# Performance work log

Measured on AMD Instinct MI355X. Metric: run time of the kernel, lower is better.

Reference implementation:

```python
import jax, jax.numpy as jnp
import numpy as np

MAX_RADIUS = 0.9
TEMP = 0.1

def _to_poincare(x, W, b):
    # Linear + Tanh, then rescale into Poincare ball of radius 0.9
    h = jnp.tanh(x @ W.T + b)
    norm = jnp.clip(jnp.linalg.norm(h, axis=-1, keepdims=True), 1e-8, None)
    scale = jnp.where(norm > MAX_RADIUS, MAX_RADIUS / norm, jnp.ones_like(norm))
    return h * scale

def setup_inputs() -> dict:
    key = jax.random.key(0)
    kq, kw, kb, km, ko = jax.random.split(key, 5)
    B, N, D = 2048, 100000, 128
    return {
        "query": jax.random.normal(kq, (B, D), dtype=jnp.float32),
        "W": jax.random.normal(kw, (D, D), dtype=jnp.float32) * (1.0 / np.sqrt(D)),
        "b": jax.random.normal(kb, (D,), dtype=jnp.float32) * 0.01,
        "mem_emb": jax.random.normal(km, (N, D), dtype=jnp.float32),
        "mem_out": jax.random.normal(ko, (N, D), dtype=jnp.float32),
        "k": 16,
    }

def reference(query, W, b, mem_emb, mem_out, k):
    q = _to_poincare(query, W, b)          # [B, D]
    m = _to_poincare(mem_emb, W, b)        # [N, D]
    # Euclidean cdist via the GEMM form: ||q||^2 + ||m||^2 - 2 q.m
    q2 = jnp.sum(q * q, axis=-1, keepdims=True)           # [B, 1]
    m2 = jnp.sum(m * m, axis=-1)                          # [N]
    d2 = q2 + m2[None, :] - 2.0 * (q @ m.T)               # [B, N]
    dists = jnp.sqrt(jnp.maximum(d2, 1e-12))
    # k smallest distances
    neg_top, top_idx = jax.lax.top_k(-dists, k)           # [B, k]
    top_dists = -neg_top
    weights = jax.nn.softmax(-top_dists / TEMP, axis=-1)  # [B, k]
    outcomes = mem_out[top_idx]                           # [B, k, D]
    return weights, outcomes
```

## Files before the change

### kernel.cpp

```cpp
#include <hip/hip_runtime.h>
#include <hip/hip_bf16.h>
#include <math.h>

#define DIM 128
#define QB 64
#define MB 128
#define NSPLIT 16
#define KSEL 16
#define KOWN 4
#define RESCORE 32
#define IDXMASK 0x1FFFu
#define KEYMASK 0xFFFFE000u

using bf16x8 = __attribute__((ext_vector_type(8))) short;
using f32x4  = __attribute__((ext_vector_type(4))) float;

__device__ inline unsigned short f2bf(float f) {
  __hip_bfloat16 h = __float2bfloat16(f);
  return __builtin_bit_cast(unsigned short, h);
}

__device__ inline f32x4 mfma16(bf16x8 a, bf16x8 b, f32x4 c) {
  return __builtin_amdgcn_mfma_f32_16x16x32_bf16(a, b, c, 0, 0, 0);
}

__device__ inline void gload_lds16(const void* g, void* l) {
  __builtin_amdgcn_global_load_lds(
      (const __attribute__((address_space(1))) void*)g,
      (__attribute__((address_space(3))) void*)l, 16, 0, 0);
}

__global__ __launch_bounds__(512) void poincare2_k(
    const float* __restrict__ Xm, int Rm,
    const float* __restrict__ Xq, int Rq,
    const float* __restrict__ W, const float* __restrict__ bias,
    float* __restrict__ Pm, float* __restrict__ Pm2,
    unsigned short* __restrict__ Pmbf,
    float* __restrict__ Pq, float* __restrict__ Pq2, int nbm)
{
  __shared__ float Wl[DIM * DIM];
  __shared__ float nrm[128 * 17];
  __shared__ float norm2l[128];

  const int t  = threadIdx.x;
  const int cg = t & 15;
  const int rg = t >> 4;

  const bool ismem = (int)blockIdx.x < nbm;
  const float* X = ismem ? Xm : Xq;
  const int    R = ismem ? Rm : Rq;
  float*       P  = ismem ? Pm  : Pq;
  float*       P2 = ismem ? Pm2 : Pq2;
  unsigned short* Pbf = ismem ? Pmbf : nullptr;
  const int rbase = (ismem ? blockIdx.x : (blockIdx.x - nbm)) * 128;

  for (int i = t; i < DIM * 32; i += 512) {
    const int j = i >> 5, c = i & 31;
    const float4 v = *(const float4*)&W[j * DIM + c * 4];
    *(float4*)&Wl[j * DIM + ((c ^ ((j >> 3) & 7)) << 2)] = v;
  }
  float bj[8];
  #pragma unroll
  for (int u = 0; u < 8; ++u) bj[u] = bias[cg * 8 + u];

  const float* xr[4];
  #pragma unroll
  for (int v = 0; v < 4; ++v) {
    int row = rbase + rg + 32 * v;
    if (row > R - 1) row = R - 1;
    xr[v] = X + (size_t)row * DIM;
  }
  __syncthreads();

  float acc[4][8];
  #pragma unroll
  for (int v = 0; v < 4; ++v)
    #pragma unroll
    for (int u = 0; u < 8; ++u) acc[v][u] = bj[u];

  #pragma unroll 2
  for (int k4 = 0; k4 < 32; ++k4) {
    float4 xv[4], wv[8];
    #pragma unroll
    for (int v = 0; v < 4; ++v) xv[v] = *(const float4*)&xr[v][k4 * 4];
    #pragma unroll
    for (int u = 0; u < 8; ++u) {
      const int j = cg * 8 + u;
      wv[u] = *(const float4*)&Wl[j * DIM + ((k4 ^ ((j >> 3) & 7)) << 2)];
    }
    #pragma unroll
    for (int v = 0; v < 4; ++v)
      #pragma unroll
      for (int u = 0; u < 8; ++u) {
        acc[v][u] = fmaf(xv[v].x, wv[u].x, acc[v][u]);
        acc[v][u] = fmaf(xv[v].y, wv[u].y, acc[v][u]);
        acc[v][u] = fmaf(xv[v].z, wv[u].z, acc[v][u]);
        acc[v][u] = fmaf(xv[v].w, wv[u].w, acc[v][u]);
      }
  }

  #pragma unroll
  for (int v = 0; v < 4; ++v) {
    float pn = 0.f;
    #pragma unroll
    for (int u = 0; u < 8; ++u) {
      const float th = tanhf(acc[v][u]);
      acc[v][u] = th;
      pn = fmaf(th, th, pn);
    }
    nrm[(rg + 32 * v) * 17 + cg] = pn;
  }
  __syncthreads();
  if (t < 128) {
    float s = 0.f;
    #pragma unroll
    for (int c2 = 0; c2 < 16; ++c2) s += nrm[t * 17 + c2];
    norm2l[t] = s;
    if (rbase + t < R) {
      const float nm = sqrtf(s);
      const float sc = (nm > 0.9f) ? (0.9f / nm) : 1.0f;
      P2[rbase + t] = s * sc * sc;
    }
  }
  __syncthreads();

  #pragma unroll
  for (int v = 0; v < 4; ++v) {
    const int r = rg + 32 * v;
    const int row = rbase + r;
    if (row < R) {
      const float n2 = norm2l[r];
      const float nm = sqrtf(n2);
      const float sc = (nm > 0.9f) ? (0.9f / nm) : 1.0f;
      float o[8];
      #pragma unroll
      for (int u = 0; u < 8; ++u) o[u] = acc[v][u] * sc;
      *(float4*)&P[(size_t)row * DIM + cg * 8]     = make_float4(o[0], o[1], o[2], o[3]);
      *(float4*)&P[(size_t)row * DIM + cg * 8 + 4] = make_float4(o[4], o[5], o[6], o[7]);
      if (Pbf) {
        uint4 pb;
        pb.x = (unsigned)f2bf(o[0]) | ((unsigned)f2bf(o[1]) << 16);
        pb.y = (unsigned)f2bf(o[2]) | ((unsigned)f2bf(o[3]) << 16);
        pb.z = (unsigned)f2bf(o[4]) | ((unsigned)f2bf(o[5]) << 16);
        pb.w = (unsigned)f2bf(o[6]) | ((unsigned)f2bf(o[7]) << 16);
        *(uint4*)&Pmbf[(size_t)row * DIM + ((cg ^ (row & 7)) << 3)] = pb;
      }
    }
  }
}

template<bool USEBF>
__global__ __launch_bounds__(512, 4) void score_topk_k(
    const float* __restrict__ Pq,
    const float* __restrict__ Pm, const float* __restrict__ Pm2,
    const unsigned short* __restrict__ Pmbf,
    int N, int splitlen, unsigned* __restrict__ splitTop)
{
  __shared__ __align__(16) unsigned short Ml[2][MB * DIM];
  __shared__ float m2p2l[2][MB];

  const int t = threadIdx.x;
  const int lane = t & 63;
  const int w = t >> 6, wr = w >> 2, wc = w & 3;
  const int split = blockIdx.x;
  const int qbase = blockIdx.y * QB;
  const int mlo = split * splitlen;
  const int mhi = min(mlo + splitlen, N);

  bf16x8 qf[2][4];
  #pragma unroll
  for (int s = 0; s < 2; ++s) {
    const int qrow = qbase + (wr * 2 + s) * 16 + (lane & 15);
    #pragma unroll
    for (int ks = 0; ks < 4; ++ks) {
      const float* src = &Pq[(size_t)qrow * DIM + ks * 32 + (lane >> 4) * 8];
      float4 lo = *(const float4*)src;
      float4 hi = *(const float4*)(src + 4);
      bf16x8 v;
      v[0] = (short)f2bf(lo.x); v[1] = (short)f2bf(lo.y);
      v[2] = (short)f2bf(lo.z); v[3] = (short)f2bf(lo.w);
      v[4] = (short)f2bf(hi.x); v[5] = (short)f2bf(hi.y);
      v[6] = (short)f2bf(hi.z); v[7] = (short)f2bf(hi.w);
      qf[s][ks] = v;
    }
  }

  uint4 sv[4];
  auto stage_issue = [&](int mbase, int buf) {
    if constexpr (USEBF) {
      #pragma unroll
      for (int i = 0; i < 4; ++i) {
        const int rr = w * 16 + i * 4;
        const unsigned short* src = Pmbf +
            (size_t)(mbase + rr + (lane >> 4)) * DIM + ((lane & 15) << 3);
        gload_lds16(src, &Ml[buf][rr * DIM]);
      }
    } else {
      const int r = t >> 2, qt = t & 3;
      const float* src = Pm + (size_t)(mbase + r) * DIM + qt * 32;
      #pragma unroll
      for (int u = 0; u < 4; ++u) {
        float4 a = *(const float4*)(src + u * 8);
        float4 b = *(const float4*)(src + u * 8 + 4);
        uint4 o;
        o.x = (unsigned)f2bf(a.x) | ((unsigned)f2bf(a.y) << 16);
        o.y = (unsigned)f2bf(a.z) | ((unsigned)f2bf(a.w) << 16);
        o.z = (unsigned)f2bf(b.x) | ((unsigned)f2bf(b.y) << 16);
        o.w = (unsigned)f2bf(b.z) | ((unsigned)f2bf(b.w) << 16);
        sv[u] = o;
      }
    }
  };
  auto stage_write_fb = [&](int buf) {
    if constexpr (!USEBF) {
      const int r = t >> 2, qt = t & 3;
      char* base = (char*)&Ml[buf][0] + r * 256;
      #pragma unroll
      for (int u = 0; u < 4; ++u)
        *(uint4*)(base + (((qt * 4 + u) ^ (r & 7)) << 4)) = sv[u];
    }
  };

  float m2n = __int_as_float(0x7f800000);
  stage_issue(mlo, 0);
  if (t < MB) {
    const int gr = mlo + t;
    if (gr < mhi) m2n = Pm2[gr] + 2.0f;
  }
  stage_write_fb(0);
  if (t < MB) m2p2l[0][t] = m2n;
  __syncthreads();

  unsigned keys[2][4][KOWN];
  #pragma unroll
  for (int s = 0; s < 2; ++s)
    #pragma unroll
    for (int r = 0; r < 4; ++r)
      #pragma unroll
      for (int i = 0; i < KOWN; ++i) keys[s][r][i] = 0xFFFFFFFFu;

  const int ntiles = (mhi - mlo + MB - 1) / MB;

  for (int tile = 0; tile < ntiles; ++tile) {
    const int cur = tile & 1;
    const bool more = (tile + 1 < ntiles);

    if (more) {
      stage_issue(mlo + (tile + 1) * MB, cur ^ 1);
      m2n = __int_as_float(0x7f800000);
      if (t < MB) {
        const int gr = mlo + (tile + 1) * MB + t;
        if (gr < mhi) m2n = Pm2[gr] + 2.0f;
      }
    }

    const float m2a = m2p2l[cur][wc * 32 + (lane & 15)];
    const float m2b = m2p2l[cur][wc * 32 + 16 + (lane & 15)];

    f32x4 acc[2][2];
    #pragma unroll
    for (int s = 0; s < 2; ++s)
      #pragma unroll
      for (int n = 0; n < 2; ++n) acc[s][n] = (f32x4){0.f, 0.f, 0.f, 0.f};

    __builtin_amdgcn_s_setprio(1);
    #pragma unroll
    for (int ks = 0; ks < 4; ++ks) {
      #pragma unroll
      for (int n = 0; n < 2; ++n) {
        const int row = (wc * 2 + n) * 16 + (lane & 15);
        const int cb  = (ks * 64 + (lane >> 4) * 16) ^ ((row & 7) << 4);
        bf16x8 bfr = *(const bf16x8*)((const char*)&Ml[cur][0] + row * 256 + cb);
        acc[0][n] = mfma16(qf[0][ks], bfr, acc[0][n]);
        acc[1][n] = mfma16(qf[1][ks], bfr, acc[1][n]);
      }
    }
    __builtin_amdgcn_s_setprio(0);

    const unsigned ibase = (unsigned)(tile * MB + wc * 32 + (lane & 15));
    #pragma unroll
    for (int s = 0; s < 2; ++s)
      #pragma unroll
      for (int n = 0; n < 2; ++n) {
        const float m2v = n ? m2b : m2a;
        const unsigned idxn = ibase + n * 16;
        #pragma unroll
        for (int r = 0; r < 4; ++r) {
          const float d2 = fmaf(-2.0f, acc[s][n][r], m2v);
          unsigned c = (__float_as_uint(d2) & KEYMASK) | idxn;
          #pragma unroll
          for (int i = 0; i < KOWN; ++i) {
            const unsigned lo = c < keys[s][r][i] ? c : keys[s][r][i];
            c = c < keys[s][r][i] ? keys[s][r][i] : c;
            keys[s][r][i] = lo;
          }
        }
      }

    if (more) {
      stage_write_fb(cur ^ 1);
      if (t < MB) m2p2l[cur ^ 1][t] = m2n;
    }
    __syncthreads();
  }

  #pragma unroll
  for (int s = 0; s < 2; ++s)
    #pragma unroll
    for (int r = 0; r < 4; ++r) {
      unsigned k0 = keys[s][r][0], k1 = keys[s][r][1];
      unsigned k2 = keys[s][r][2], k3 = keys[s][r][3];
      unsigned out = 0xFFFFFFFFu;
      for (int round = 0; round < 8; ++round) {
        unsigned g = k0, o;
        o = __shfl_xor(g, 1, 16); g = o < g ? o : g;
        o = __shfl_xor(g, 2, 16); g = o < g ? o : g;
        o = __shfl_xor(g, 4, 16); g = o < g ? o : g;
        o = __shfl_xor(g, 8, 16); g = o < g ? o : g;
        const bool mine = (k0 == g);
        k0 = mine ? k1 : k0;
        k1 = mine ? k2 : k1;
        k2 = mine ? k3 : k2;
        k3 = mine ? 0xFFFFFFFFu : k3;
        if ((lane & 15) == round) out = g;
      }
      const int q = qbase + wr * 32 + s * 16 + (lane >> 4) * 4 + r;
      if ((lane & 15) < 8)
        splitTop[(((size_t)q * NSPLIT + split) * 4 + wc) * 8 + (lane & 15)] = out;
    }
}

__global__ __launch_bounds__(256) void finalize_k(
    const unsigned* __restrict__ splitTop,
    const float* __restrict__ Pq, const float* __restrict__ Pq2,
    const float* __restrict__ Pm, const float* __restrict__ Pm2,
    const float* __restrict__ memOut, int N, int splitlen,
    float* __restrict__ outW, float* __restrict__ outO)
{
  const int q = blockIdx.x;
  const int t = threadIdx.x;
  __shared__ unsigned selKey[RESCORE];
  __shared__ int      selSrc[RESCORE];
  __shared__ unsigned long long keyx[RESCORE];
  __shared__ unsigned long long selB[KSEL];
  __shared__ float el[KSEL];

  if (t < 64) {
    const unsigned* gp = splitTop + (size_t)q * (NSPLIT * 4 * 8) + t * 8;
    unsigned k0 = gp[0], k1 = gp[1], k2 = gp[2], k3 = gp[3];
    unsigned k4 = gp[4], k5 = gp[5], k6 = gp[6], k7 = gp[7];
    for (int r = 0; r < RESCORE; ++r) {
      unsigned g = k0, o;
      #pragma unroll
      for (int st = 1; st < 64; st <<= 1) { o = __shfl_xor(g, st); g = o < g ? o : g; }
      unsigned long long mask = __ballot(k0 == g);
      const int fl = __ffsll((unsigned long long)mask) - 1;
      if (t == fl) {
        selKey[r] = g;
        selSrc[r] = t;
        k0 = k1; k1 = k2; k2 = k3; k3 = k4;
        k4 = k5; k5 = k6; k6 = k7; k7 = 0xFFFFFFFFu;
      }
    }
  }
  __syncthreads();

  {
    const int g = t >> 3, e = t & 7;
    const int gidx = (selSrc[g] >> 2) * splitlen + (int)(selKey[g] & IDXMASK);
    const float4* qr = (const float4*)&Pq[(size_t)q * DIM];
    const float4* mr = (const float4*)&Pm[(size_t)gidx * DIM];
    float s = 0.f;
    #pragma unroll
    for (int u = 0; u < 4; ++u) {
      float4 a = qr[e * 4 + u], b = mr[e * 4 + u];
      s = fmaf(a.x, b.x, s); s = fmaf(a.y, b.y, s);
      s = fmaf(a.z, b.z, s); s = fmaf(a.w, b.w, s);
    }
    s += __shfl_xor(s, 1, 8);
    s += __shfl_xor(s, 2, 8);
    s += __shfl_xor(s, 4, 8);
    if (e == 0) {
      float d2 = (Pq2[q] + Pm2[gidx]) - 2.0f * s;
      float dist = sqrtf(fmaxf(d2, 1e-12f));
      keyx[g] = (((unsigned long long)__float_as_uint(dist)) << 32) | (unsigned)gidx;
    }
  }
  __syncthreads();

  if (t < 64) {
    unsigned long long kk = (t < RESCORE) ? keyx[t] : ~0ull;
    for (int r = 0; r < KSEL; ++r) {
      unsigned long long g = kk;
      #pragma unroll
      for (int o = 1; o < 64; o <<= 1) {
        unsigned long long s = __shfl_xor(g, o);
        g = (s < g) ? s : g;
      }
      if (kk == g) kk = ~0ull;
      if (t == 0) selB[r] = g;
    }
  }
  __syncthreads();

  if (t < KSEL) {
    const float d  = __uint_as_float((unsigned)(selB[t] >> 32));
    const float d0 = __uint_as_float((unsigned)(selB[0] >> 32));
    el[t] = expf(-(d / 0.1f) + (d0 / 0.1f));
  }
  __syncthreads();
  if (t < KSEL) {
    float sum = 0.f;
    #pragma unroll
    for (int i = 0; i < KSEL; ++i) sum += el[i];
    outW[(size_t)q * KSEL + t] = el[t] / sum;
  }

  for (int f4 = t; f4 < KSEL * 32; f4 += 256) {
    int r = f4 >> 5, c4 = f4 & 31;
    int idx = (int)(selB[r] & 0xffffffffu);
    *(float4*)&outO[((size_t)q * KSEL + r) * DIM + c4 * 4] =
        *(const float4*)&memOut[(size_t)idx * DIM + c4 * 4];
  }
}

extern "C" void kernel_launch(void* const* d_in, const int* in_sizes, int n_in,
                              void* d_out, int out_size, void* d_ws, size_t ws_size,
                              hipStream_t stream)
{
  const float* query   = (const float*)d_in[0];
  const float* W       = (const float*)d_in[1];
  const float* bias    = (const float*)d_in[2];
  const float* mem_emb = (const float*)d_in[3];
  const float* mem_out = (const float*)d_in[4];
  const int B = in_sizes[0] / DIM;
  const int N = in_sizes[3] / DIM;
  const int N_pad = ((N + MB + 15) / 16) * 16;

  const int splitlen = ((N + NSPLIT * MB - 1) / (NSPLIT * MB)) * MB;

  float* ws  = (float*)d_ws;
  float* Pm  = ws;
  float* Pm2 = Pm + (size_t)N_pad * DIM;
  float* Pq  = Pm2 + N_pad;
  float* Pq2 = Pq + (size_t)B * DIM;
  unsigned* splitTop = (unsigned*)(Pq2 + B);
  unsigned short* Pmbf = (unsigned short*)(splitTop + (size_t)B * NSPLIT * 4 * 8);
  const size_t need_bf = (size_t)((char*)(Pmbf + (size_t)N_pad * DIM) - (char*)d_ws);
  const bool usebf = ws_size >= need_bf;

  float* outW = (float*)d_out;
  float* outO = outW + (size_t)B * KSEL;

  const int nbm = (N + 127) / 128;
  const int nbq = (B + 127) / 128;
  poincare2_k<<<dim3(nbm + nbq), dim3(512), 0, stream>>>(
      mem_emb, N, query, B, W, bias, Pm, Pm2, usebf ? Pmbf : nullptr, Pq, Pq2, nbm);

  dim3 grid2(NSPLIT, B / QB);
  if (usebf)
    score_topk_k<true><<<grid2, dim3(512), 0, stream>>>(Pq, Pm, Pm2, Pmbf, N,
                                                        splitlen, splitTop);
  else
    score_topk_k<false><<<grid2, dim3(512), 0, stream>>>(Pq, Pm, Pm2, nullptr, N,
                                                         splitlen, splitTop);

  finalize_k<<<dim3(B), dim3(256), 0, stream>>>(splitTop, Pq, Pq2, Pm, Pm2,
                                                mem_out, N, splitlen, outW, outO);
}
```

Measured before the change: 228.6 us.

## Halve score tile, double splits, swap grid order, merge two key lists in finalize

The scoring kernel now stages 64 memory rows per tile instead of 128, uses 32 splits instead of 16, and raises launch bounds to 8 blocks per SM. The grid order is swapped so query blocks vary fastest, and the loop is unrolled into explicit double-buffer bodies. Finalize merges two per-thread sorted candidate lists, since twice as many split outputs now arrive per query. This aims for more parallelism and occupancy, at the cost of halving the memory tile reused per query fragment load, more sync barriers, and a larger merge.

```diff
diff --git a/kernel.cpp b/kernel.cpp
--- a/kernel.cpp
+++ b/kernel.cpp
@@ -4,8 +4,8 @@
 
 #define DIM 128
 #define QB 64
-#define MB 128
-#define NSPLIT 16
+#define MB 64
+#define NSPLIT 32
 #define KSEL 16
 #define KOWN 4
 #define RESCORE 32
@@ -143,27 +143,28 @@
         pb.y = (unsigned)f2bf(o[2]) | ((unsigned)f2bf(o[3]) << 16);
         pb.z = (unsigned)f2bf(o[4]) | ((unsigned)f2bf(o[5]) << 16);
         pb.w = (unsigned)f2bf(o[6]) | ((unsigned)f2bf(o[7]) << 16);
-        *(uint4*)&Pmbf[(size_t)row * DIM + ((cg ^ (row & 7)) << 3)] = pb;
+        *(uint4*)&Pbf[(size_t)row * DIM + ((cg ^ (row & 7)) << 3)] = pb;
       }
     }
   }
 }
 
 template<bool USEBF>
-__global__ __launch_bounds__(512, 4) void score_topk_k(
+__global__ __launch_bounds__(512, 8) void score_topk_k(
     const float* __restrict__ Pq,
     const float* __restrict__ Pm, const float* __restrict__ Pm2,
     const unsigned short* __restrict__ Pmbf,
     int N, int splitlen, unsigned* __restrict__ splitTop)
 {
-  __shared__ __align__(16) unsigned short Ml[2][MB * DIM];
-  __shared__ float m2p2l[2][MB];
+  __shared__ __align__(16) unsigned short Ml0[MB * DIM];
+  __shared__ __align__(16) unsigned short Ml1[MB * DIM];
+  __shared__ float m20[MB], m21[MB];
 
   const int t = threadIdx.x;
   const int lane = t & 63;
   const int w = t >> 6, wr = w >> 2, wc = w & 3;
-  const int split = blockIdx.x;
-  const int qbase = blockIdx.y * QB;
+  const int qbase = blockIdx.x * QB;
+  const int split = blockIdx.y;
   const int mlo = split * splitlen;
   const int mhi = min(mlo + splitlen, N);
 
@@ -185,50 +186,49 @@
     }
   }
 
-  uint4 sv[4];
-  auto stage_issue = [&](int mbase, int buf) {
+  const size_t soff0 = (size_t)(w * 8 + (lane >> 4)) * DIM + ((lane & 15) << 3);
+  const size_t soff1 = soff0 + 4 * DIM;
+  unsigned short* const d00 = &Ml0[(w * 8) * DIM];
+  unsigned short* const d01 = &Ml0[(w * 8 + 4) * DIM];
+  unsigned short* const d10 = &Ml1[(w * 8) * DIM];
+  unsigned short* const d11 = &Ml1[(w * 8 + 4) * DIM];
+
+  auto stage = [&](int mbase, unsigned short* dA, unsigned short* dB,
+                   unsigned short* lds) {
     if constexpr (USEBF) {
-      #pragma unroll
-      for (int i = 0; i < 4; ++i) {
-        const int rr = w * 16 + i * 4;
-        const unsigned short* src = Pmbf +
-            (size_t)(mbase + rr + (lane >> 4)) * DIM + ((lane & 15) << 3);
-        gload_lds16(src, &Ml[buf][rr * DIM]);
-      }
+      const unsigned short* b = Pmbf + (size_t)mbase * DIM;
+      gload_lds16(b + soff0, dA);
+      gload_lds16(b + soff1, dB);
     } else {
-      const int r = t >> 2, qt = t & 3;
-      const float* src = Pm + (size_t)(mbase + r) * DIM + qt * 32;
-      #pragma unroll
-      for (int u = 0; u < 4; ++u) {
-        float4 a = *(const float4*)(src + u * 8);
-        float4 b = *(const float4*)(src + u * 8 + 4);
-        uint4 o;
-        o.x = (unsigned)f2bf(a.x) | ((unsigned)f2bf(a.y) << 16);
-        o.y = (unsigned)f2bf(a.z) | ((unsigned)f2bf(a.w) << 16);
-        o.z = (unsigned)f2bf(b.x) | ((unsigned)f2bf(b.y) << 16);
-        o.w = (unsigned)f2bf(b.z) | ((unsigned)f2bf(b.w) << 16);
-        sv[u] = o;
-      }
+      const int fr = t >> 3, fe = t & 7;
+      const float* src = Pm + (size_t)(mbase + fr) * DIM + fe * 16;
+      float4 a0 = *(const float4*)(src + 0);
+      float4 a1 = *(const float4*)(src + 4);
+      float4 a2 = *(const float4*)(src + 8);
+      float4 a3 = *(const float4*)(src + 12);
+      uint4 o0, o1;
+      o0.x = (unsigned)f2bf(a0.x) | ((unsigned)f2bf(a0.y) << 16);
+      o0.y = (unsigned)f2bf(a0.z) | ((unsigned)f2bf(a0.w) << 16);
+      o0.z = (unsigned)f2bf(a1.x) | ((unsigned)f2bf(a1.y) << 16);
+      o0.w = (unsigned)f2bf(a1.z) | ((unsigned)f2bf(a1.w) << 16);
+      o1.x = (unsigned)f2bf(a2.x) | ((unsigned)f2bf(a2.y) << 16);
+      o1.y = (unsigned)f2bf(a2.z) | ((unsigned)f2bf(a2.w) << 16);
+      o1.z = (unsigned)f2bf(a3.x) | ((unsigned)f2bf(a3.y) << 16);
+      o1.w = (unsigned)f2bf(a3.z) | ((unsigned)f2bf(a3.w) << 16);
+      char* base = (char*)lds + fr * 256;
+      *(uint4*)(base + (((2 * fe)     ^ (fr & 7)) << 4)) = o0;
+      *(uint4*)(base + (((2 * fe + 1) ^ (fr & 7)) << 4)) = o1;
     }
   };
-  auto stage_write_fb = [&](int buf) {
-    if constexpr (!USEBF) {
-      const int r = t >> 2, qt = t & 3;
-      char* base = (char*)&Ml[buf][0] + r * 256;
-      #pragma unroll
-      for (int u = 0; u < 4; ++u)
-        *(uint4*)(base + (((qt * 4 + u) ^ (r & 7)) << 4)) = sv[u];
-    }
-  };
-
-  float m2n = __int_as_float(0x7f800000);
-  stage_issue(mlo, 0);
+
+  const int ntiles = (mhi - mlo + MB - 1) / MB;
+  const int mcol = wc * 16 + (lane & 15);
+
+  stage(mlo, d00, d01, Ml0);
   if (t < MB) {
     const int gr = mlo + t;
-    if (gr < mhi) m2n = Pm2[gr] + 2.0f;
-  }
-  stage_write_fb(0);
-  if (t < MB) m2p2l[0][t] = m2n;
+    m20[t] = (gr < mhi) ? (Pm2[gr] + 2.0f) : __int_as_float(0x7f800000);
+  }
   __syncthreads();
 
   unsigned keys[2][4][KOWN];
@@ -239,69 +239,57 @@
       #pragma unroll
       for (int i = 0; i < KOWN; ++i) keys[s][r][i] = 0xFFFFFFFFu;
 
-  const int ntiles = (mhi - mlo + MB - 1) / MB;
-
-  for (int tile = 0; tile < ntiles; ++tile) {
-    const int cur = tile & 1;
+  auto body = [&](int tile, const unsigned short* ldsCur,
+                  unsigned short* dA, unsigned short* dB, unsigned short* ldsNxt,
+                  const float* m2cur, float* m2nxt) {
+    const int mbase = mlo + tile * MB;
     const bool more = (tile + 1 < ntiles);
-
     if (more) {
-      stage_issue(mlo + (tile + 1) * MB, cur ^ 1);
-      m2n = __int_as_float(0x7f800000);
+      stage(mbase + MB, dA, dB, ldsNxt);
       if (t < MB) {
-        const int gr = mlo + (tile + 1) * MB + t;
-        if (gr < mhi) m2n = Pm2[gr] + 2.0f;
-      }
-    }
-
-    const float m2a = m2p2l[cur][wc * 32 + (lane & 15)];
-    const float m2b = m2p2l[cur][wc * 32 + 16 + (lane & 15)];
-
-    f32x4 acc[2][2];
+        const int gr = mbase + MB + t;
+        m2nxt[t] = (gr < mhi) ? (Pm2[gr] + 2.0f) : __int_as_float(0x7f800000);
+      }
+    }
+
+    const float m2v = m2cur[mcol];
+
+    f32x4 acc[2];
+    acc[0] = (f32x4){0.f, 0.f, 0.f, 0.f};
+    acc[1] = (f32x4){0.f, 0.f, 0.f, 0.f};
+
+    const int row = wc * 16 + (lane & 15);
+    __builtin_amdgcn_s_setprio(1);
+    #pragma unroll
+    for (int ks = 0; ks < 4; ++ks) {
+      const int cb = (ks * 64 + (lane >> 4) * 16) ^ ((row & 7) << 4);
+      bf16x8 bfr = *(const bf16x8*)((const char*)ldsCur + row * 256 + cb);
+      acc[0] = mfma16(qf[0][ks], bfr, acc[0]);
+      acc[1] = mfma16(qf[1][ks], bfr, acc[1]);
+    }
+    __builtin_amdgcn_s_setprio(0);
+
+    const unsigned idxn = (unsigned)(tile * MB + mcol);
     #pragma unroll
     for (int s = 0; s < 2; ++s)
       #pragma unroll
-      for (int n = 0; n < 2; ++n) acc[s][n] = (f32x4){0.f, 0.f, 0.f, 0.f};
-
-    __builtin_amdgcn_s_setprio(1);
-    #pragma unroll
-    for (int ks = 0; ks < 4; ++ks) {
-      #pragma unroll
-      for (int n = 0; n < 2; ++n) {
-        const int row = (wc * 2 + n) * 16 + (lane & 15);
-        const int cb  = (ks * 64 + (lane >> 4) * 16) ^ ((row & 7) << 4);
-        bf16x8 bfr = *(const bf16x8*)((const char*)&Ml[cur][0] + row * 256 + cb);
-        acc[0][n] = mfma16(qf[0][ks], bfr, acc[0][n]);
-        acc[1][n] = mfma16(qf[1][ks], bfr, acc[1][n]);
-      }
-    }
-    __builtin_amdgcn_s_setprio(0);
-
-    const unsigned ibase = (unsigned)(tile * MB + wc * 32 + (lane & 15));
-    #pragma unroll
-    for (int s = 0; s < 2; ++s)
-      #pragma unroll
-      for (int n = 0; n < 2; ++n) {
-        const float m2v = n ? m2b : m2a;
-        const unsigned idxn = ibase + n * 16;
+      for (int r = 0; r < 4; ++r) {
+        const float d2 = fmaf(-2.0f, acc[s][r], m2v);
+        unsigned c = (__float_as_uint(d2) & KEYMASK) | idxn;
         #pragma unroll
-        for (int r = 0; r < 4; ++r) {
-          const float d2 = fmaf(-2.0f, acc[s][n][r], m2v);
-          unsigned c = (__float_as_uint(d2) & KEYMASK) | idxn;
-          #pragma unroll
-          for (int i = 0; i < KOWN; ++i) {
-            const unsigned lo = c < keys[s][r][i] ? c : keys[s][r][i];
-            c = c < keys[s][r][i] ? keys[s][r][i] : c;
-            keys[s][r][i] = lo;
-          }
+        for (int i = 0; i < KOWN; ++i) {
+          const unsigned lo = c < keys[s][r][i] ? c : keys[s][r][i];
+          c = c < keys[s][r][i] ? keys[s][r][i] : c;
+          keys[s][r][i] = lo;
         }
       }
-
-    if (more) {
-      stage_write_fb(cur ^ 1);
-      if (t < MB) m2p2l[cur ^ 1][t] = m2n;
-    }
     __syncthreads();
+  };
+
+  int tile = 0;
+  while (true) {
+    body(tile, Ml0, d10, d11, Ml1, m20, m21); if (++tile == ntiles) break;
+    body(tile, Ml1, d00, d01, Ml0, m21, m20); if (++tile == ntiles) break;
   }
 
   #pragma unroll
@@ -346,20 +334,30 @@
   __shared__ float el[KSEL];
 
   if (t < 64) {
-    const unsigned* gp = splitTop + (size_t)q * (NSPLIT * 4 * 8) + t * 8;
-    unsigned k0 = gp[0], k1 = gp[1], k2 = gp[2], k3 = gp[3];
-    unsigned k4 = gp[4], k5 = gp[5], k6 = gp[6], k7 = gp[7];
+    const unsigned* gp = splitTop + (size_t)q * (NSPLIT * 4 * 8) + t * 16;
+    unsigned a[8], c[8];
+    #pragma unroll
+    for (int i = 0; i < 8; ++i) { a[i] = gp[i]; c[i] = gp[8 + i]; }
     for (int r = 0; r < RESCORE; ++r) {
-      unsigned g = k0, o;
+      const unsigned myhead = a[0] < c[0] ? a[0] : c[0];
+      unsigned g = myhead, o;
       #pragma unroll
       for (int st = 1; st < 64; st <<= 1) { o = __shfl_xor(g, st); g = o < g ? o : g; }
-      unsigned long long mask = __ballot(k0 == g);
+      unsigned long long mask = __ballot(myhead == g);
       const int fl = __ffsll((unsigned long long)mask) - 1;
       if (t == fl) {
         selKey[r] = g;
-        selSrc[r] = t;
-        k0 = k1; k1 = k2; k2 = k3; k3 = k4;
-        k4 = k5; k5 = k6; k6 = k7; k7 = 0xFFFFFFFFu;
+        if (a[0] == g) {
+          selSrc[r] = 2 * t;
+          #pragma unroll
+          for (int i = 0; i < 7; ++i) a[i] = a[i + 1];
+          a[7] = 0xFFFFFFFFu;
+        } else {
+          selSrc[r] = 2 * t + 1;
+          #pragma unroll
+          for (int i = 0; i < 7; ++i) c[i] = c[i + 1];
+          c[7] = 0xFFFFFFFFu;
+        }
       }
     }
   }
@@ -457,7 +455,7 @@
   poincare2_k<<<dim3(nbm + nbq), dim3(512), 0, stream>>>(
       mem_emb, N, query, B, W, bias, Pm, Pm2, usebf ? Pmbf : nullptr, Pq, Pq2, nbm);
 
-  dim3 grid2(NSPLIT, B / QB);
+  dim3 grid2(B / QB, NSPLIT);
   if (usebf)
     score_topk_k<true><<<grid2, dim3(512), 0, stream>>>(Pq, Pm, Pm2, Pmbf, N,
                                                         splitlen, splitTop);
```

After: 740.5 us. +224.0%, slower.
